# Kernel optimization log

Measured on AMD Instinct MI355X. Metric: run time of the kernel, lower is better.

## Reference

```python
import jax, jax.numpy as jnp
import numpy as np

H = 8     # n_head_qk == n_head_v
DF = 32   # d_fix_qk == d_fix_v

def setup_inputs() -> dict:
    key = jax.random.key(0)
    k0, k1, k2, k3, k4 = jax.random.split(key, 5)
    x = jax.random.normal(k0, (2, 2048, 128), jnp.float32)
    attn_bias = jax.random.normal(k1, (1, H, 2048, 2048), jnp.float32) * 0.1
    Wqkv = jax.random.normal(k2, (3 * H * DF, 128), jnp.float32) * 0.02   # nn.Linear(d_model, 3*h*df)
    Wtalk = jax.random.normal(k3, (H, H), jnp.float32) * 0.1              # 1x1 Conv2d over head channels
    Wproj = jax.random.normal(k4, (128, H * DF), jnp.float32) * 0.02      # nn.Linear(h*df_v, d_model)
    return {"x": x, "attn_bias": attn_bias, "Wqkv": Wqkv, "Wtalk": Wtalk, "Wproj": Wproj}

def reference(x, attn_bias, Wqkv, Wtalk, Wproj):
    B, P, D = x.shape
    # qkv: [B,P,3*H*DF] -> [3,B,H,P,DF]
    qkv = (x @ Wqkv.T).reshape(B, P, 3, H, DF).transpose(2, 0, 3, 1, 4)
    scale = jnp.sqrt(jnp.asarray(DF, x.dtype))
    q, k, v = qkv[0] / scale, qkv[1], qkv[2]
    attn = jnp.einsum('bhpd,bhqd->bhpq', q, k)          # [B,H,P,P]
    attn = jnp.einsum('gh,bhpq->bgpq', Wtalk, attn)     # talking-heads 1x1 conv
    attn = jax.nn.softmax(attn + attn_bias, axis=-1)
    out = jnp.einsum('bhpq,bhqd->bhpd', attn, v)        # [B,H,P,DF]
    out = out.transpose(0, 2, 1, 3).reshape(B, P, H * DF)
    return out @ Wproj.T                                 # [B,P,D]
```

## Files before the change

### kernel.cpp

```cpp
#include <hip/hip_runtime.h>


typedef __attribute__((ext_vector_type(8))) short short8v;
typedef __attribute__((ext_vector_type(4))) float f32x4;

static __device__ __forceinline__ unsigned short f2bf(float f) {
  union { float f; unsigned u; } v; v.f = f;
  return (unsigned short)((v.u + 0x7FFFu + ((v.u >> 16) & 1u)) >> 16);
}

static __device__ __forceinline__ void load_lds_128(const void* g, void* lp) {
  __builtin_amdgcn_global_load_lds(
      (const __attribute__((address_space(1))) void*)g,
      (__attribute__((address_space(3))) void*)lp, 16, 0, 0);
}

__global__ __launch_bounds__(256) void qkv_kernel(
    const float* __restrict__ x, const float* __restrict__ Wqkv,
    unsigned short* __restrict__ q_ws, unsigned short* __restrict__ k_ws,
    unsigned short* __restrict__ v_t) {
  __shared__ float xl[8][128];
  const int tid = threadIdx.x;
  const int rowbase = blockIdx.x * 8;
  {
    int r = tid >> 5, k4 = (tid & 31) * 4;
    *(float4*)&xl[r][k4] = *(const float4*)&x[(size_t)(rowbase + r) * 128 + k4];
  }
  __syncthreads();
  float acc[8][3];
#pragma unroll
  for (int r = 0; r < 8; ++r) { acc[r][0] = 0.f; acc[r][1] = 0.f; acc[r][2] = 0.f; }
  const float* w0p = &Wqkv[(size_t)tid * 128];
  const float* w1p = &Wqkv[(size_t)(tid + 256) * 128];
  const float* w2p = &Wqkv[(size_t)(tid + 512) * 128];
  for (int k4 = 0; k4 < 128; k4 += 4) {
    float4 w0 = *(const float4*)&w0p[k4];
    float4 w1 = *(const float4*)&w1p[k4];
    float4 w2 = *(const float4*)&w2p[k4];
#pragma unroll
    for (int r = 0; r < 8; ++r) {
      float4 xv = *(const float4*)&xl[r][k4];
      acc[r][0] += xv.x * w0.x + xv.y * w0.y + xv.z * w0.z + xv.w * w0.w;
      acc[r][1] += xv.x * w1.x + xv.y * w1.y + xv.z * w1.z + xv.w * w1.w;
      acc[r][2] += xv.x * w2.x + xv.y * w2.y + xv.z * w2.z + xv.w * w2.w;
    }
  }
  const int h = tid >> 5, d = tid & 31;
#pragma unroll
  for (int r = 0; r < 8; ++r) {
    int row = rowbase + r, b = row >> 11, pp = row & 2047;
    size_t base = ((size_t)(b * 8 + h) * 2048 + pp) * 32 + d;
    q_ws[base] = f2bf(acc[r][0] * 0.17677669529663687f);
    k_ws[base] = f2bf(acc[r][1]);
    v_t[((size_t)(b * 8 + h) * 32 + d) * 2048 + pp] = f2bf(acc[r][2]);
  }
}

#define RAW_BARRIER() do { \
  asm volatile("s_waitcnt lgkmcnt(0)" ::: "memory"); \
  __builtin_amdgcn_sched_barrier(0); \
  __builtin_amdgcn_s_barrier(); \
  __builtin_amdgcn_sched_barrier(0); \
} while (0)

#define FULL_BARRIER() do { \
  asm volatile("s_waitcnt vmcnt(0) lgkmcnt(0)" ::: "memory"); \
  __builtin_amdgcn_sched_barrier(0); \
  __builtin_amdgcn_s_barrier(); \
  __builtin_amdgcn_sched_barrier(0); \
} while (0)

#define STAGE_KV(BUF, KQ) do { \
  _Pragma("unroll") \
  for (int i_ = 0; i_ < 4; ++i_) { \
    int c_ = w * 4 + i_; int hc_ = c_ >> 1; int sc_ = c_ & 1; \
    load_lds_128(&k_ws[((size_t)((b * 8 + hc_) * 2048) + (KQ) + sc_ * 16 + ln) * 32 + lg * 8], \
                 &Kb[BUF][c_ * 512]); \
    load_lds_128(&v_t[((size_t)((b * 8 + hc_) * 32) + sc_ * 16 + ln) * 2048 + (KQ) + lg * 8], \
                 &Vb[BUF][c_ * 512]); \
  } \
} while (0)

#define BIAS_LOAD(BREG, KQ) do { \
  _Pragma("unroll") \
  for (int g_ = 0; g_ < 8; ++g_) \
    BREG[g_] = *(const float4*)&bias[(size_t)g_ * 4194304 + (size_t)prow * 2048 + (KQ) + qs * 4]; \
} while (0)

#define BODY(S, CUR, BC, BN) do { \
  FULL_BARRIER();  \
  const int kq0_ = kv0 + (S) * 32; \
  if ((S) + 1 < 32) { STAGE_KV(1 - (CUR), kq0_ + 32); } \
   \
  _Pragma("unroll") \
  for (int hh = 0; hh < 2; ++hh) { \
    const int h_ = 2 * w + hh; \
    _Pragma("unroll") \
    for (int qt = 0; qt < 2; ++qt) { \
      short8v kf = *(const short8v*)&Kb[CUR][(size_t)(h_ * 2 + qt) * 512 + l * 8]; \
      _Pragma("unroll") \
      for (int pt = 0; pt < 2; ++pt) { \
        f32x4 s4 = __builtin_amdgcn_mfma_f32_16x16x32_bf16( \
            qf[hh][pt], kf, (f32x4){0.f, 0.f, 0.f, 0.f}, 0, 0, 0); \
        _Pragma("unroll") \
        for (int r = 0; r < 4; ++r) \
          Sb[h_ * 1088 + (pt * 16 + lg * 4 + r) * 32 + qt * 16 + ln] = s4[r]; \
      } \
    } \
  } \
  RAW_BARRIER();  \
  {  \
    float4 sv[8]; \
    _Pragma("unroll") \
    for (int h = 0; h < 8; ++h) sv[h] = *(const float4*)&Sb[h * 1088 + p_mix * 32 + qs * 4]; \
    if ((S) + 1 < 32) { BIAS_LOAD(BN, kq0_ + 32); } \
    _Pragma("unroll") \
    for (int g = 0; g < 8; ++g) { \
      float4 t4 = BC[g]; \
      _Pragma("unroll") \
      for (int h = 0; h < 8; ++h) { \
        const float wgh = wt[g * 8 + h]; \
        t4.x += wgh * sv[h].x; t4.y += wgh * sv[h].y; \
        t4.z += wgh * sv[h].z; t4.w += wgh * sv[h].w; \
      } \
      float mx = fmaxf(fmaxf(t4.x, t4.y), fmaxf(t4.z, t4.w)); \
      mx = fmaxf(mx, __shfl_xor(mx, 1)); \
      mx = fmaxf(mx, __shfl_xor(mx, 2)); \
      mx = fmaxf(mx, __shfl_xor(mx, 4)); \
      const float mnew = fmaxf(mreg[g], mx); \
      const float a_ = __expf(mreg[g] - mnew); \
      mreg[g] = mnew; \
      float ex = __expf(t4.x - mnew), ey = __expf(t4.y - mnew); \
      float ez = __expf(t4.z - mnew), ew = __expf(t4.w - mnew); \
      float ls = ex + ey + ez + ew; \
      ls += __shfl_xor(ls, 1); ls += __shfl_xor(ls, 2); ls += __shfl_xor(ls, 4); \
      lreg[g] = lreg[g] * a_ + ls; \
      if (qs == 0) Sb[g * 1088 + 1024 + p_mix] = a_;  \
      unsigned u0 = (unsigned)f2bf(ex) | ((unsigned)f2bf(ey) << 16); \
      unsigned u1 = (unsigned)f2bf(ez) | ((unsigned)f2bf(ew) << 16); \
      uint2 pk; pk.x = u0; pk.y = u1; \
      *(uint2*)&Pb[(size_t)((g * 2 + (p_mix >> 4)) * 64 + (qs >> 1) * 16 + (p_mix & 15)) * 8 + (qs & 1) * 4] = pk; \
    } \
  } \
  RAW_BARRIER();  \
   \
  _Pragma("unroll") \
  for (int hh = 0; hh < 2; ++hh) { \
    const int h_ = 2 * w + hh; \
    _Pragma("unroll") \
    for (int pt = 0; pt < 2; ++pt) { \
      float4 av = *(const float4*)&Sb[h_ * 1088 + 1024 + pt * 16 + lg * 4]; \
      short8v pa = *(const short8v*)&Pb[(size_t)((h_ * 2 + pt) * 64 + l) * 8]; \
      _Pragma("unroll") \
      for (int dt = 0; dt < 2; ++dt) { \
        f32x4 o = Of[hh][pt][dt]; \
        o[0] *= av.x; o[1] *= av.y; o[2] *= av.z; o[3] *= av.w; \
        short8v vf = *(const short8v*)&Vb[CUR][(size_t)(h_ * 2 + dt) * 512 + l * 8]; \
        Of[hh][pt][dt] = __builtin_amdgcn_mfma_f32_16x16x32_bf16(pa, vf, o, 0, 0, 0); \
      } \
    } \
  } \
} while (0)

__global__ __launch_bounds__(256, 1) void attn_kernel(
    const unsigned short* __restrict__ q_ws, const unsigned short* __restrict__ k_ws,
    const unsigned short* __restrict__ v_t, const float* __restrict__ bias,
    const float* __restrict__ Wtalk, float* __restrict__ pm, float* __restrict__ pl,
    float* __restrict__ pO) {
  __shared__ __align__(16) unsigned short Kb[2][8192];
  __shared__ __align__(16) unsigned short Vb[2][8192];
  __shared__ __align__(16) float Sb[8 * 1088];
  __shared__ __align__(16) unsigned short Pb[8192];

  const int qt_blk = blockIdx.x, split = blockIdx.y, b = blockIdx.z;
  const int q0 = qt_blk * 32, kv0 = split * 1024;
  const int tid = threadIdx.x, w = tid >> 6, l = tid & 63, lg = l >> 4, ln = l & 15;
  const int p_mix = tid >> 3, qs = tid & 7, prow = q0 + p_mix;

  float wt[64];
#pragma unroll
  for (int i = 0; i < 64; ++i) wt[i] = Wtalk[i];

  short8v qf[2][2];
#pragma unroll
  for (int hh = 0; hh < 2; ++hh)
#pragma unroll
    for (int pt = 0; pt < 2; ++pt) {
      int h = 2 * w + hh;
      size_t a = ((size_t)((b * 8 + h) * 2048) + q0 + pt * 16 + ln) * 32 + lg * 8;
      qf[hh][pt] = *(const short8v*)&q_ws[a];
    }

  f32x4 Of[2][2][2];
#pragma unroll
  for (int hh = 0; hh < 2; ++hh)
#pragma unroll
    for (int pt = 0; pt < 2; ++pt)
#pragma unroll
      for (int dt = 0; dt < 2; ++dt) Of[hh][pt][dt] = (f32x4){0.f, 0.f, 0.f, 0.f};

  float mreg[8], lreg[8];
#pragma unroll
  for (int g = 0; g < 8; ++g) { mreg[g] = -1e30f; lreg[g] = 0.f; }

  float4 BA[8], BB[8];
  STAGE_KV(0, kv0);
  BIAS_LOAD(BA, kv0);

  for (int s2 = 0; s2 < 16; ++s2) {
    BODY(2 * s2, 0, BA, BB);
    BODY(2 * s2 + 1, 1, BB, BA);
  }

  const size_t ob = (size_t)((split * 2 + b) * 8);
#pragma unroll
  for (int hh = 0; hh < 2; ++hh)
#pragma unroll
    for (int pt = 0; pt < 2; ++pt)
#pragma unroll
      for (int dt = 0; dt < 2; ++dt)
#pragma unroll
        for (int r = 0; r < 4; ++r) {
          int h = 2 * w + hh;
          size_t idx = ((ob + h) * 2048 + q0 + pt * 16 + lg * 4 + r) * 32 + dt * 16 + ln;
          pO[idx] = Of[hh][pt][dt][r];
        }
  if (qs == 0) {
#pragma unroll
    for (int g = 0; g < 8; ++g) {
      size_t idx = (ob + g) * 2048 + prow;
      pm[idx] = mreg[g];
      pl[idx] = lreg[g];
    }
  }
}

__global__ __launch_bounds__(256) void comb_kernel(
    const float* __restrict__ pm, const float* __restrict__ pl,
    const float* __restrict__ pO, const float* __restrict__ Wproj,
    float* __restrict__ out) {
  __shared__ float ol[8][256];
  const int tid = threadIdx.x;
  const int rowbase = blockIdx.x * 8;
  {
    const int g = tid >> 5, d = tid & 31;
    for (int r = 0; r < 8; ++r) {
      int row = rowbase + r, b = row >> 11, p = row & 2047;
      size_t b0 = ((size_t)(b * 8 + g) * 2048 + p);
      float m0 = pm[b0], m1 = pm[b0 + 32768];
      float l0 = pl[b0], l1 = pl[b0 + 32768];
      float mx = fmaxf(m0, m1);
      float w0 = __expf(m0 - mx), w1 = __expf(m1 - mx);
      float o0 = pO[b0 * 32 + d], o1 = pO[(b0 + 32768) * 32 + d];
      ol[r][tid] = (o0 * w0 + o1 * w1) / (l0 * w0 + l1 * w1);
    }
  }
  __syncthreads();
  const int j = tid & 127, rh = tid >> 7;
  float acc[8];
#pragma unroll
  for (int r = 0; r < 8; ++r) acc[r] = 0.f;
  for (int c4 = 0; c4 < 128; c4 += 4) {
    float4 wv = *(const float4*)&Wproj[(size_t)j * 256 + rh * 128 + c4];
#pragma unroll
    for (int r = 0; r < 8; ++r) {
      float4 ov = *(const float4*)&ol[r][rh * 128 + c4];
      acc[r] += ov.x * wv.x + ov.y * wv.y + ov.z * wv.z + ov.w * wv.w;
    }
  }
  __syncthreads();
  float* red = &ol[0][0];
#pragma unroll
  for (int r = 0; r < 8; ++r) red[(r * 128 + j) * 2 + rh] = acc[r];
  __syncthreads();
#pragma unroll
  for (int rr = 0; rr < 4; ++rr) {
    int r = (tid >> 7) * 4 + rr;
    int row = rowbase + r;
    out[(size_t)row * 128 + (tid & 127)] =
        red[(r * 128 + (tid & 127)) * 2] + red[(r * 128 + (tid & 127)) * 2 + 1];
  }
}

extern "C" void kernel_launch(void* const* d_in, const int* in_sizes, int n_in,
                              void* d_out, int out_size, void* d_ws, size_t ws_size,
                              hipStream_t stream) {
  const float* x     = (const float*)d_in[0];
  const float* bias  = (const float*)d_in[1];
  const float* Wqkv  = (const float*)d_in[2];
  const float* Wtalk = (const float*)d_in[3];
  const float* Wproj = (const float*)d_in[4];
  float* out = (float*)d_out;
  char* ws = (char*)d_ws;
  unsigned short* q_ws = (unsigned short*)(ws);
  unsigned short* k_ws = (unsigned short*)(ws + (2u << 20));
  unsigned short* v_t  = (unsigned short*)(ws + (4u << 20));
  float* pm = (float*)(ws + (6u << 20));
  float* pl = (float*)(ws + (6u << 20) + 262144);
  float* pO = (float*)(ws + (7u << 20));

  qkv_kernel<<<512, 256, 0, stream>>>(x, Wqkv, q_ws, k_ws, v_t);
  attn_kernel<<<dim3(64, 2, 2), 256, 0, stream>>>(q_ws, k_ws, v_t, bias, Wtalk, pm, pl, pO);
  comb_kernel<<<512, 256, 0, stream>>>(pm, pl, pO, Wproj, out);
}
```

Before: 360.5 us.

## Raise KV split count, load K/V fragments directly into registers, allow two blocks/CU

The attention kernel now splits the KV range into up to 8 chunks, chosen from the workspace size, so far more blocks are launched (1024 instead of 256 on a 256-CU-class GPU). The LDS double-buffered K/V staging via global_load_lds is replaced by per-lane register prefetch of K/V fragments and bias for the next step, and launch bounds allow 2 blocks per CU. The combine kernel is generalized to merge SPLIT partials. This targets low occupancy and underused CUs, at the cost of more partial-output traffic and a heavier combine step.

New measurement: 316.3 us. 12.2% less time.

```diff
diff --git a/kernel.cpp b/kernel.cpp
--- a/kernel.cpp
+++ b/kernel.cpp
@@ -9,11 +9,12 @@
   return (unsigned short)((v.u + 0x7FFFu + ((v.u >> 16) & 1u)) >> 16);
 }
 
-static __device__ __forceinline__ void load_lds_128(const void* g, void* lp) {
-  __builtin_amdgcn_global_load_lds(
-      (const __attribute__((address_space(1))) void*)g,
-      (__attribute__((address_space(3))) void*)lp, 16, 0, 0);
-}
+#define RAW_BARRIER() do { \
+  asm volatile("s_waitcnt lgkmcnt(0)" ::: "memory"); \
+  __builtin_amdgcn_sched_barrier(0); \
+  __builtin_amdgcn_s_barrier(); \
+  __builtin_amdgcn_sched_barrier(0); \
+} while (0)
 
 __global__ __launch_bounds__(256) void qkv_kernel(
     const float* __restrict__ x, const float* __restrict__ Wqkv,
@@ -56,124 +57,18 @@
   }
 }
 
-#define RAW_BARRIER() do { \
-  asm volatile("s_waitcnt lgkmcnt(0)" ::: "memory"); \
-  __builtin_amdgcn_sched_barrier(0); \
-  __builtin_amdgcn_s_barrier(); \
-  __builtin_amdgcn_sched_barrier(0); \
-} while (0)
-
-#define FULL_BARRIER() do { \
-  asm volatile("s_waitcnt vmcnt(0) lgkmcnt(0)" ::: "memory"); \
-  __builtin_amdgcn_sched_barrier(0); \
-  __builtin_amdgcn_s_barrier(); \
-  __builtin_amdgcn_sched_barrier(0); \
-} while (0)
-
-#define STAGE_KV(BUF, KQ) do { \
-  _Pragma("unroll") \
-  for (int i_ = 0; i_ < 4; ++i_) { \
-    int c_ = w * 4 + i_; int hc_ = c_ >> 1; int sc_ = c_ & 1; \
-    load_lds_128(&k_ws[((size_t)((b * 8 + hc_) * 2048) + (KQ) + sc_ * 16 + ln) * 32 + lg * 8], \
-                 &Kb[BUF][c_ * 512]); \
-    load_lds_128(&v_t[((size_t)((b * 8 + hc_) * 32) + sc_ * 16 + ln) * 2048 + (KQ) + lg * 8], \
-                 &Vb[BUF][c_ * 512]); \
-  } \
-} while (0)
-
-#define BIAS_LOAD(BREG, KQ) do { \
-  _Pragma("unroll") \
-  for (int g_ = 0; g_ < 8; ++g_) \
-    BREG[g_] = *(const float4*)&bias[(size_t)g_ * 4194304 + (size_t)prow * 2048 + (KQ) + qs * 4]; \
-} while (0)
-
-#define BODY(S, CUR, BC, BN) do { \
-  FULL_BARRIER();  \
-  const int kq0_ = kv0 + (S) * 32; \
-  if ((S) + 1 < 32) { STAGE_KV(1 - (CUR), kq0_ + 32); } \
-   \
-  _Pragma("unroll") \
-  for (int hh = 0; hh < 2; ++hh) { \
-    const int h_ = 2 * w + hh; \
-    _Pragma("unroll") \
-    for (int qt = 0; qt < 2; ++qt) { \
-      short8v kf = *(const short8v*)&Kb[CUR][(size_t)(h_ * 2 + qt) * 512 + l * 8]; \
-      _Pragma("unroll") \
-      for (int pt = 0; pt < 2; ++pt) { \
-        f32x4 s4 = __builtin_amdgcn_mfma_f32_16x16x32_bf16( \
-            qf[hh][pt], kf, (f32x4){0.f, 0.f, 0.f, 0.f}, 0, 0, 0); \
-        _Pragma("unroll") \
-        for (int r = 0; r < 4; ++r) \
-          Sb[h_ * 1088 + (pt * 16 + lg * 4 + r) * 32 + qt * 16 + ln] = s4[r]; \
-      } \
-    } \
-  } \
-  RAW_BARRIER();  \
-  {  \
-    float4 sv[8]; \
-    _Pragma("unroll") \
-    for (int h = 0; h < 8; ++h) sv[h] = *(const float4*)&Sb[h * 1088 + p_mix * 32 + qs * 4]; \
-    if ((S) + 1 < 32) { BIAS_LOAD(BN, kq0_ + 32); } \
-    _Pragma("unroll") \
-    for (int g = 0; g < 8; ++g) { \
-      float4 t4 = BC[g]; \
-      _Pragma("unroll") \
-      for (int h = 0; h < 8; ++h) { \
-        const float wgh = wt[g * 8 + h]; \
-        t4.x += wgh * sv[h].x; t4.y += wgh * sv[h].y; \
-        t4.z += wgh * sv[h].z; t4.w += wgh * sv[h].w; \
-      } \
-      float mx = fmaxf(fmaxf(t4.x, t4.y), fmaxf(t4.z, t4.w)); \
-      mx = fmaxf(mx, __shfl_xor(mx, 1)); \
-      mx = fmaxf(mx, __shfl_xor(mx, 2)); \
-      mx = fmaxf(mx, __shfl_xor(mx, 4)); \
-      const float mnew = fmaxf(mreg[g], mx); \
-      const float a_ = __expf(mreg[g] - mnew); \
-      mreg[g] = mnew; \
-      float ex = __expf(t4.x - mnew), ey = __expf(t4.y - mnew); \
-      float ez = __expf(t4.z - mnew), ew = __expf(t4.w - mnew); \
-      float ls = ex + ey + ez + ew; \
-      ls += __shfl_xor(ls, 1); ls += __shfl_xor(ls, 2); ls += __shfl_xor(ls, 4); \
-      lreg[g] = lreg[g] * a_ + ls; \
-      if (qs == 0) Sb[g * 1088 + 1024 + p_mix] = a_;  \
-      unsigned u0 = (unsigned)f2bf(ex) | ((unsigned)f2bf(ey) << 16); \
-      unsigned u1 = (unsigned)f2bf(ez) | ((unsigned)f2bf(ew) << 16); \
-      uint2 pk; pk.x = u0; pk.y = u1; \
-      *(uint2*)&Pb[(size_t)((g * 2 + (p_mix >> 4)) * 64 + (qs >> 1) * 16 + (p_mix & 15)) * 8 + (qs & 1) * 4] = pk; \
-    } \
-  } \
-  RAW_BARRIER();  \
-   \
-  _Pragma("unroll") \
-  for (int hh = 0; hh < 2; ++hh) { \
-    const int h_ = 2 * w + hh; \
-    _Pragma("unroll") \
-    for (int pt = 0; pt < 2; ++pt) { \
-      float4 av = *(const float4*)&Sb[h_ * 1088 + 1024 + pt * 16 + lg * 4]; \
-      short8v pa = *(const short8v*)&Pb[(size_t)((h_ * 2 + pt) * 64 + l) * 8]; \
-      _Pragma("unroll") \
-      for (int dt = 0; dt < 2; ++dt) { \
-        f32x4 o = Of[hh][pt][dt]; \
-        o[0] *= av.x; o[1] *= av.y; o[2] *= av.z; o[3] *= av.w; \
-        short8v vf = *(const short8v*)&Vb[CUR][(size_t)(h_ * 2 + dt) * 512 + l * 8]; \
-        Of[hh][pt][dt] = __builtin_amdgcn_mfma_f32_16x16x32_bf16(pa, vf, o, 0, 0, 0); \
-      } \
-    } \
-  } \
-} while (0)
-
-__global__ __launch_bounds__(256, 1) void attn_kernel(
+template <int SPLIT>
+__global__ __launch_bounds__(256, 2) void attn_kernel(
     const unsigned short* __restrict__ q_ws, const unsigned short* __restrict__ k_ws,
     const unsigned short* __restrict__ v_t, const float* __restrict__ bias,
     const float* __restrict__ Wtalk, float* __restrict__ pm, float* __restrict__ pl,
     float* __restrict__ pO) {
-  __shared__ __align__(16) unsigned short Kb[2][8192];
-  __shared__ __align__(16) unsigned short Vb[2][8192];
+  constexpr int NB = 64 / SPLIT;
   __shared__ __align__(16) float Sb[8 * 1088];
   __shared__ __align__(16) unsigned short Pb[8192];
 
   const int qt_blk = blockIdx.x, split = blockIdx.y, b = blockIdx.z;
-  const int q0 = qt_blk * 32, kv0 = split * 1024;
+  const int q0 = qt_blk * 32, kv0 = split * (2048 / SPLIT);
   const int tid = threadIdx.x, w = tid >> 6, l = tid & 63, lg = l >> 4, ln = l & 15;
   const int p_mix = tid >> 3, qs = tid & 7, prow = q0 + p_mix;
 
@@ -203,13 +98,126 @@
 #pragma unroll
   for (int g = 0; g < 8; ++g) { mreg[g] = -1e30f; lreg[g] = 0.f; }
 
-  float4 BA[8], BB[8];
-  STAGE_KV(0, kv0);
-  BIAS_LOAD(BA, kv0);
-
-  for (int s2 = 0; s2 < 16; ++s2) {
-    BODY(2 * s2, 0, BA, BB);
-    BODY(2 * s2 + 1, 1, BB, BA);
+  const unsigned short *kB[2][2], *vB[2][2];
+#pragma unroll
+  for (int hh = 0; hh < 2; ++hh)
+#pragma unroll
+    for (int sc = 0; sc < 2; ++sc) {
+      kB[hh][sc] = k_ws + ((size_t)(b * 8 + 2 * w + hh) * 2048 + kv0 + sc * 16 + ln) * 32 + lg * 8;
+      vB[hh][sc] = v_t + ((size_t)(b * 8 + 2 * w + hh) * 32 + sc * 16 + ln) * 2048 + kv0 + lg * 8;
+    }
+  const float* bB = bias + (size_t)prow * 2048 + kv0 + qs * 4;
+
+  short8v kf[2][2], vf[2][2];
+  float4 bf[8];
+#pragma unroll
+  for (int hh = 0; hh < 2; ++hh)
+#pragma unroll
+    for (int sc = 0; sc < 2; ++sc) {
+      kf[hh][sc] = *(const short8v*)kB[hh][sc];
+      vf[hh][sc] = *(const short8v*)vB[hh][sc];
+    }
+#pragma unroll
+  for (int g = 0; g < 8; ++g) bf[g] = *(const float4*)(bB + (size_t)g * 4194304);
+
+#pragma unroll 2
+  for (int s = 0; s < NB; ++s) {
+    const int sn = (s + 1 < NB) ? s + 1 : s;
+
+#pragma unroll
+    for (int hh = 0; hh < 2; ++hh) {
+      const int h_ = 2 * w + hh;
+#pragma unroll
+      for (int qt = 0; qt < 2; ++qt) {
+#pragma unroll
+        for (int pt = 0; pt < 2; ++pt) {
+          f32x4 s4 = __builtin_amdgcn_mfma_f32_16x16x32_bf16(
+              qf[hh][pt], kf[hh][qt], (f32x4){0.f, 0.f, 0.f, 0.f}, 0, 0, 0);
+#pragma unroll
+          for (int r = 0; r < 4; ++r)
+            Sb[h_ * 1088 + (pt * 16 + lg * 4 + r) * 32 + qt * 16 + ln] = s4[r];
+        }
+      }
+    }
+    RAW_BARRIER();
+
+    short8v kf_n[2][2];
+#pragma unroll
+    for (int hh = 0; hh < 2; ++hh)
+#pragma unroll
+      for (int sc = 0; sc < 2; ++sc)
+        kf_n[hh][sc] = *(const short8v*)(kB[hh][sc] + (size_t)sn * 1024);
+
+    {
+      float4 sv[8];
+#pragma unroll
+      for (int h = 0; h < 8; ++h)
+        sv[h] = *(const float4*)&Sb[h * 1088 + p_mix * 32 + qs * 4];
+#pragma unroll
+      for (int g = 0; g < 8; ++g) {
+        float4 t4 = bf[g];
+#pragma unroll
+        for (int h = 0; h < 8; ++h) {
+          const float wgh = wt[g * 8 + h];
+          t4.x += wgh * sv[h].x; t4.y += wgh * sv[h].y;
+          t4.z += wgh * sv[h].z; t4.w += wgh * sv[h].w;
+        }
+        float mx = fmaxf(fmaxf(t4.x, t4.y), fmaxf(t4.z, t4.w));
+        mx = fmaxf(mx, __shfl_xor(mx, 1));
+        mx = fmaxf(mx, __shfl_xor(mx, 2));
+        mx = fmaxf(mx, __shfl_xor(mx, 4));
+        const float mnew = fmaxf(mreg[g], mx);
+        const float a_ = __expf(mreg[g] - mnew);
+        mreg[g] = mnew;
+        float ex = __expf(t4.x - mnew), ey = __expf(t4.y - mnew);
+        float ez = __expf(t4.z - mnew), ew = __expf(t4.w - mnew);
+        float ls = ex + ey + ez + ew;
+        ls += __shfl_xor(ls, 1); ls += __shfl_xor(ls, 2); ls += __shfl_xor(ls, 4);
+        lreg[g] = lreg[g] * a_ + ls;
+        if (qs == 0) Sb[g * 1088 + 1024 + p_mix] = a_;
+        unsigned u0 = (unsigned)f2bf(ex) | ((unsigned)f2bf(ey) << 16);
+        unsigned u1 = (unsigned)f2bf(ez) | ((unsigned)f2bf(ew) << 16);
+        uint2 pk; pk.x = u0; pk.y = u1;
+        *(uint2*)&Pb[(size_t)((g * 2 + (p_mix >> 4)) * 64 + (qs >> 1) * 16 + (p_mix & 15)) * 8 + (qs & 1) * 4] = pk;
+      }
+    }
+
+    float4 bf_n[8];
+#pragma unroll
+    for (int g = 0; g < 8; ++g)
+      bf_n[g] = *(const float4*)(bB + (size_t)g * 4194304 + sn * 32);
+
+    RAW_BARRIER();
+
+#pragma unroll
+    for (int hh = 0; hh < 2; ++hh) {
+      const int h_ = 2 * w + hh;
+#pragma unroll
+      for (int pt = 0; pt < 2; ++pt) {
+        float4 av = *(const float4*)&Sb[h_ * 1088 + 1024 + pt * 16 + lg * 4];
+        short8v pa = *(const short8v*)&Pb[(size_t)((h_ * 2 + pt) * 64 + l) * 8];
+#pragma unroll
+        for (int dt = 0; dt < 2; ++dt) {
+          f32x4 o = Of[hh][pt][dt];
+          o[0] *= av.x; o[1] *= av.y; o[2] *= av.z; o[3] *= av.w;
+          Of[hh][pt][dt] = __builtin_amdgcn_mfma_f32_16x16x32_bf16(pa, vf[hh][dt], o, 0, 0, 0);
+        }
+      }
+    }
+
+    short8v vf_n[2][2];
+#pragma unroll
+    for (int hh = 0; hh < 2; ++hh)
+#pragma unroll
+      for (int sc = 0; sc < 2; ++sc)
+        vf_n[hh][sc] = *(const short8v*)(vB[hh][sc] + sn * 32);
+
+#pragma unroll
+    for (int hh = 0; hh < 2; ++hh)
+#pragma unroll
+      for (int sc = 0; sc < 2; ++sc) { kf[hh][sc] = kf_n[hh][sc]; vf[hh][sc] = vf_n[hh][sc]; }
+#pragma unroll
+    for (int g = 0; g < 8; ++g) bf[g] = bf_n[g];
   }
 
   const size_t ob = (size_t)((split * 2 + b) * 8);
@@ -235,6 +243,7 @@
   }
 }
 
+template <int SPLIT>
 __global__ __launch_bounds__(256) void comb_kernel(
     const float* __restrict__ pm, const float* __restrict__ pl,
     const float* __restrict__ pO, const float* __restrict__ Wproj,
@@ -247,12 +256,21 @@
     for (int r = 0; r < 8; ++r) {
       int row = rowbase + r, b = row >> 11, p = row & 2047;
       size_t b0 = ((size_t)(b * 8 + g) * 2048 + p);
-      float m0 = pm[b0], m1 = pm[b0 + 32768];
-      float l0 = pl[b0], l1 = pl[b0 + 32768];
-      float mx = fmaxf(m0, m1);
-      float w0 = __expf(m0 - mx), w1 = __expf(m1 - mx);
-      float o0 = pO[b0 * 32 + d], o1 = pO[(b0 + 32768) * 32 + d];
-      ol[r][tid] = (o0 * w0 + o1 * w1) / (l0 * w0 + l1 * w1);
+      float ms[SPLIT];
+      float mx = -1e30f;
+#pragma unroll
+      for (int s = 0; s < SPLIT; ++s) {
+        ms[s] = pm[b0 + (size_t)s * 32768];
+        mx = fmaxf(mx, ms[s]);
+      }
+      float den = 0.f, acc = 0.f;
+#pragma unroll
+      for (int s = 0; s < SPLIT; ++s) {
+        float ww = __expf(ms[s] - mx);
+        den += ww * pl[b0 + (size_t)s * 32768];
+        acc += ww * pO[(b0 + (size_t)s * 32768) * 32 + d];
+      }
+      ol[r][tid] = acc / den;
     }
   }
   __syncthreads();
@@ -295,11 +313,24 @@
   unsigned short* q_ws = (unsigned short*)(ws);
   unsigned short* k_ws = (unsigned short*)(ws + (2u << 20));
   unsigned short* v_t  = (unsigned short*)(ws + (4u << 20));
-  float* pm = (float*)(ws + (6u << 20));
-  float* pl = (float*)(ws + (6u << 20) + 262144);
-  float* pO = (float*)(ws + (7u << 20));
+
+  const size_t base = 6291456;
+  const size_t per_split = 4456448;
+  int SPLIT = (ws_size >= base + 8 * per_split) ? 8
+            : (ws_size >= base + 4 * per_split) ? 4 : 2;
+  float* pm = (float*)(ws + base);
+  float* pl = (float*)(ws + base + (size_t)SPLIT * 131072);
+  float* pO = (float*)(ws + base + (size_t)SPLIT * 262144);
 
   qkv_kernel<<<512, 256, 0, stream>>>(x, Wqkv, q_ws, k_ws, v_t);
-  attn_kernel<<<dim3(64, 2, 2), 256, 0, stream>>>(q_ws, k_ws, v_t, bias, Wtalk, pm, pl, pO);
-  comb_kernel<<<512, 256, 0, stream>>>(pm, pl, pO, Wproj, out);
-}
+  if (SPLIT == 8) {
+    attn_kernel<8><<<dim3(64, 8, 2), 256, 0, stream>>>(q_ws, k_ws, v_t, bias, Wtalk, pm, pl, pO);
+    comb_kernel<8><<<512, 256, 0, stream>>>(pm, pl, pO, Wproj, out);
+  } else if (SPLIT == 4) {
+    attn_kernel<4><<<dim3(64, 4, 2), 256, 0, stream>>>(q_ws, k_ws, v_t, bias, Wtalk, pm, pl, pO);
+    comb_kernel<4><<<512, 256, 0, stream>>>(pm, pl, pO, Wproj, out);
+  } else {
+    attn_kernel<2><<<dim3(64, 2, 2), 256, 0, stream>>>(q_ws, k_ws, v_t, bias, Wtalk, pm, pl, pO);
+    comb_kernel<2><<<512, 256, 0, stream>>>(pm, pl, pO, Wproj, out);
+  }
+}
```
